# Kernel optimization log

Measured on AMD Instinct MI355X. Metric: run time of the kernel, lower is better.

The kernel has to match this reference:

```python
import jax, jax.numpy as jnp
import numpy as np

NODE_ATOM = 64   # nodes per graph (fixed by layer3 Linear(1*node_atom, n_h1))
N_H1 = 1024
DIM_OUT = 128
N_NODES = 524288          # 8192 graphs * 64 nodes
N_EDGES = 16777216        # avg degree 32
BN_EPS = 1e-5


def setup_inputs() -> dict:
    key = jax.random.key(0)
    ks = jax.random.split(key, 16)
    x = jax.random.normal(ks[0], (N_NODES, 1), dtype=jnp.float32)
    edge_attr = jax.random.uniform(ks[1], (N_EDGES, 1), dtype=jnp.float32)
    edge_index = jax.random.randint(ks[2], (2, N_EDGES), 0, N_NODES, dtype=jnp.int64)
    # CGConv gated MLP params: lin_f, lin_s : Linear(2*1+1=3 -> 1)
    cg_wf = jax.random.normal(ks[3], (1, 3), dtype=jnp.float32) * 0.5
    cg_bf = jax.random.normal(ks[4], (1,), dtype=jnp.float32) * 0.1
    cg_ws = jax.random.normal(ks[5], (1, 3), dtype=jnp.float32) * 0.5
    cg_bs = jax.random.normal(ks[6], (1,), dtype=jnp.float32) * 0.1
    # GCNConv(1,1)
    gcn_w = jax.random.normal(ks[7], (1, 1), dtype=jnp.float32)
    gcn_b = jax.random.normal(ks[8], (1,), dtype=jnp.float32) * 0.1
    # MLP head
    l3_w = jax.random.normal(ks[9], (N_H1, NODE_ATOM), dtype=jnp.float32) / np.sqrt(NODE_ATOM)
    l3_b = jax.random.normal(ks[10], (N_H1,), dtype=jnp.float32) * 0.1
    bn_gamma = jnp.ones((N_H1,), dtype=jnp.float32)
    bn_beta = jnp.zeros((N_H1,), dtype=jnp.float32)
    l4_w = jax.random.normal(ks[11], (DIM_OUT, N_H1), dtype=jnp.float32) / np.sqrt(N_H1)
    l4_b = jax.random.normal(ks[12], (DIM_OUT,), dtype=jnp.float32) * 0.1
    return {"x": x, "edge_attr": edge_attr, "cg_wf": cg_wf, "cg_bf": cg_bf,
            "cg_ws": cg_ws, "cg_bs": cg_bs, "gcn_w": gcn_w, "gcn_b": gcn_b,
            "l3_w": l3_w, "l3_b": l3_b, "bn_gamma": bn_gamma, "bn_beta": bn_beta,
            "l4_w": l4_w, "l4_b": l4_b, "edge_index": edge_index}


def reference(x, edge_attr, cg_wf, cg_bf, cg_ws, cg_bs, gcn_w, gcn_b,
              l3_w, l3_b, bn_gamma, bn_beta, l4_w, l4_b, edge_index):
    n = x.shape[0]
    src = edge_index[0]  # x_j (message source)
    dst = edge_index[1]  # x_i (aggregation target)

    # ---- CGConv: z = [x_i, x_j, e]; msg = sigmoid(Wf z) * softplus(Ws z); out = x + sum_j msg
    z = jnp.concatenate([x[dst], x[src], edge_attr], axis=-1)      # [E,3]
    msg = jax.nn.sigmoid(z @ cg_wf.T + cg_bf) * jax.nn.softplus(z @ cg_ws.T + cg_bs)
    h = x + jax.ops.segment_sum(msg, dst, num_segments=n)
    h = jax.nn.relu(h)  # dropout in eval mode = identity

    # ---- GCNConv(1,1, add_self_loops=False), edge_attr used as edge_weight
    w = edge_attr[:, 0]
    deg = jax.ops.segment_sum(w, dst, num_segments=n)
    dinv = jnp.where(deg > 0, 1.0 / jnp.sqrt(jnp.maximum(deg, 1e-12)), 0.0)
    norm = dinv[src] * w * dinv[dst]                               # [E]
    hw = h @ gcn_w.T                                               # [N,1]
    h = jax.ops.segment_sum(norm[:, None] * hw[src], dst, num_segments=n) + gcn_b
    h = jax.nn.relu(h)

    # ---- to_dense_batch (uniform sorted batch) + transpose + flatten == reshape [B, node_atom]
    b = n // NODE_ATOM
    h = h.reshape(b, NODE_ATOM)

    # ---- MLP head: Linear -> BatchNorm1d (eval: running mean 0, var 1) -> relu -> Linear -> relu
    h = h @ l3_w.T + l3_b
    h = bn_gamma * h / jnp.sqrt(1.0 + BN_EPS) + bn_beta
    h = jax.nn.relu(h)
    h = jax.nn.relu(h @ l4_w.T + l4_b)
    return h
```

## Files before the change

kernel.cpp:

```cpp
#include <hip/hip_runtime.h>
#include <math.h>

#define N_NODES 524288
#define N_EDGES 16777216
#define H1      1024
#define DOUT    128

#define NB        128
#define BSH       12
#define NODES_PB  4096
#define EPB       8192
#define NBLK      (N_EDGES / EPB)
#define CAP       139264
#define PWG       8

__device__ __forceinline__ float sigmoid_f(float v) {
    return 1.0f / (1.0f + __expf(-v));
}
__device__ __forceinline__ float softplus_f(float v) {
    return fmaxf(v, 0.0f) + log1pf(__expf(-fabsf(v)));
}


__global__ __launch_bounds__(1024) void a1_bin4(
    const int* __restrict__ ei, const float* __restrict__ ea,
    int* __restrict__ gcur,
    uint2* __restrict__ pkw_g)
{
    __shared__ int cnt[NB];
    __shared__ int gpos[NB];
    const int c = blockIdx.x, t = threadIdx.x;

    const int vi0 = c * 2048 + t;
    const int vi1 = vi0 + 1024;
    const int4 s4a = ((const int4*)ei)[vi0];
    const int4 s4b = ((const int4*)ei)[vi1];
    const int4 d4a = ((const int4*)(ei + N_EDGES))[vi0];
    const int4 d4b = ((const int4*)(ei + N_EDGES))[vi1];
    const float4 w4a = ((const float4*)ea)[vi0];
    const float4 w4b = ((const float4*)ea)[vi1];
    int srcs[8], dsts[8];
    float ws[8];
    srcs[0]=s4a.x; srcs[1]=s4a.y; srcs[2]=s4a.z; srcs[3]=s4a.w;
    srcs[4]=s4b.x; srcs[5]=s4b.y; srcs[6]=s4b.z; srcs[7]=s4b.w;
    dsts[0]=d4a.x; dsts[1]=d4a.y; dsts[2]=d4a.z; dsts[3]=d4a.w;
    dsts[4]=d4b.x; dsts[5]=d4b.y; dsts[6]=d4b.z; dsts[7]=d4b.w;
    ws[0]=w4a.x; ws[1]=w4a.y; ws[2]=w4a.z; ws[3]=w4a.w;
    ws[4]=w4b.x; ws[5]=w4b.y; ws[6]=w4b.z; ws[7]=w4b.w;

    if (t < NB) cnt[t] = 0;
    __syncthreads();

    int rank[8];
#pragma unroll
    for (int q = 0; q < 8; ++q)
        rank[q] = atomicAdd(&cnt[dsts[q] >> BSH], 1);
    __syncthreads();

    if (t < NB) gpos[t] = atomicAdd(&gcur[t * 16], cnt[t]);
    __syncthreads();

#pragma unroll
    for (int q = 0; q < 8; ++q) {
        const int dst = dsts[q];
        const int b = dst >> BSH;
        const size_t slot = (size_t)b * CAP + gpos[b] + rank[q];
        const unsigned int pk = ((unsigned int)srcs[q] << 12) |
                                (unsigned int)(dst & (NODES_PB - 1));
        pkw_g[slot] = make_uint2(pk, __float_as_uint(ws[q]));
    }
}

__global__ __launch_bounds__(512) void b1_accum(
    const uint2* __restrict__ pkw_g, const int* __restrict__ gcur,
    const float* __restrict__ x,
    const float* __restrict__ cg_wf, const float* __restrict__ cg_bf,
    const float* __restrict__ cg_ws, const float* __restrict__ cg_bs,
    float* __restrict__ part1)
{
    __shared__ float lm[NODES_PB];
    __shared__ float ld[NODES_PB];
    const int b = blockIdx.x / PWG, p = blockIdx.x % PWG;
    for (int i = threadIdx.x; i < NODES_PB; i += 512) { lm[i] = 0.0f; ld[i] = 0.0f; }
    __syncthreads();
    const float wf0 = cg_wf[0], wf1 = cg_wf[1], wf2 = cg_wf[2], bf = cg_bf[0];
    const float s0c = cg_ws[0], s1c = cg_ws[1], s2c = cg_ws[2], bsc = cg_bs[0];
    const float* xb = x + (size_t)b * NODES_PB;
    const int tot = gcur[b * 16];
    const int per = (((tot + PWG - 1) / PWG) + 1) & ~1;
    const int s0 = p * per;
    const int s1 = min(tot, s0 + per);
    const uint2* base = pkw_g + (size_t)b * CAP;
    if (s1 > s0) {
        const int npair = (s1 - s0) >> 1;
        const uint4* v4 = (const uint4*)(base + s0);
#pragma unroll 2
        for (int k = threadIdx.x; k < npair; k += 512) {
            const uint4 r = v4[k];
            const int dl0 = r.x & (NODES_PB - 1), src0 = r.x >> BSH;
            const int dl1 = r.z & (NODES_PB - 1), src1 = r.z >> BSH;
            const float w0 = __uint_as_float(r.y), w1 = __uint_as_float(r.w);
            const float xs0 = x[src0], xs1 = x[src1];
            const float xd0 = xb[dl0], xd1 = xb[dl1];
            const float f0 = fmaf(wf0, xd0, fmaf(wf1, xs0, fmaf(wf2, w0, bf)));
            const float g0 = fmaf(s0c, xd0, fmaf(s1c, xs0, fmaf(s2c, w0, bsc)));
            const float f1 = fmaf(wf0, xd1, fmaf(wf1, xs1, fmaf(wf2, w1, bf)));
            const float g1 = fmaf(s0c, xd1, fmaf(s1c, xs1, fmaf(s2c, w1, bsc)));
            const float m0 = sigmoid_f(f0) * softplus_f(g0);
            const float m1 = sigmoid_f(f1) * softplus_f(g1);
            atomicAdd(&lm[dl0], m0);
            atomicAdd(&ld[dl0], w0);
            atomicAdd(&lm[dl1], m1);
            atomicAdd(&ld[dl1], w1);
        }
        for (int k = s0 + (npair << 1) + (int)threadIdx.x; k < s1; k += 512) {
            const uint2 v = base[k];
            const int dl = v.x & (NODES_PB - 1);
            const int src = v.x >> BSH;
            const float w = __uint_as_float(v.y);
            const float xs = x[src], xd = xb[dl];
            const float f = fmaf(wf0, xd, fmaf(wf1, xs, fmaf(wf2, w, bf)));
            const float g = fmaf(s0c, xd, fmaf(s1c, xs, fmaf(s2c, w, bsc)));
            atomicAdd(&lm[dl], sigmoid_f(f) * softplus_f(g));
            atomicAdd(&ld[dl], w);
        }
    }
    __syncthreads();
    float* pm = part1 + (size_t)(b * PWG + p) * NODES_PB;
    float* pd = part1 + (size_t)NB * PWG * NODES_PB + (size_t)(b * PWG + p) * NODES_PB;
    for (int k = threadIdx.x; k < NODES_PB; k += 512) { pm[k] = lm[k]; pd[k] = ld[k]; }
}

__global__ __launch_bounds__(256) void c1_nodemid(
    const float* __restrict__ part1, const float* __restrict__ x,
    const float* __restrict__ gcn_w,
    float* __restrict__ dinv, float* __restrict__ a)
{
    const int n = blockIdx.x * 256 + threadIdx.x;
    const int b = n >> BSH, dl = n & (NODES_PB - 1);
    const float* pm = part1 + (size_t)b * PWG * NODES_PB + dl;
    const float* pd = part1 + (size_t)NB * PWG * NODES_PB + (size_t)b * PWG * NODES_PB + dl;
    float m = 0.0f, d = 0.0f;
#pragma unroll
    for (int p = 0; p < PWG; ++p) {
        m += pm[(size_t)p * NODES_PB];
        d += pd[(size_t)p * NODES_PB];
    }
    const float h = fmaxf(x[n] + m, 0.0f);
    const float di = (d > 0.0f) ? (1.0f / sqrtf(fmaxf(d, 1e-12f))) : 0.0f;
    dinv[n] = di;
    a[n] = di * h * gcn_w[0];
}

__global__ __launch_bounds__(512) void b2_accum(
    const uint2* __restrict__ pkw_g, const int* __restrict__ gcur,
    const float* __restrict__ a, float* __restrict__ part2)
{
    __shared__ float ls[NODES_PB];
    const int b = blockIdx.x / PWG, p = blockIdx.x % PWG;
    for (int i = threadIdx.x; i < NODES_PB; i += 512) ls[i] = 0.0f;
    __syncthreads();
    const int tot = gcur[b * 16];
    const int per = (((tot + PWG - 1) / PWG) + 1) & ~1;
    const int s0 = p * per;
    const int s1 = min(tot, s0 + per);
    const uint2* base = pkw_g + (size_t)b * CAP;
    if (s1 > s0) {
        const int npair = (s1 - s0) >> 1;
        const uint4* v4 = (const uint4*)(base + s0);
#pragma unroll 2
        for (int k = threadIdx.x; k < npair; k += 512) {
            const uint4 r = v4[k];
            const float a0 = a[r.x >> BSH];
            const float a1 = a[r.z >> BSH];
            atomicAdd(&ls[r.x & (NODES_PB - 1)], a0 * __uint_as_float(r.y));
            atomicAdd(&ls[r.z & (NODES_PB - 1)], a1 * __uint_as_float(r.w));
        }
        for (int k = s0 + (npair << 1) + (int)threadIdx.x; k < s1; k += 512) {
            const uint2 v = base[k];
            atomicAdd(&ls[v.x & (NODES_PB - 1)], a[v.x >> BSH] * __uint_as_float(v.y));
        }
    }
    __syncthreads();
    float* ps = part2 + (size_t)(b * PWG + p) * NODES_PB;
    for (int k = threadIdx.x; k < NODES_PB; k += 512) ps[k] = ls[k];
}

__global__ __launch_bounds__(256) void c2_nodefin(
    const float* __restrict__ part2, const float* __restrict__ dinv,
    const float* __restrict__ gcn_b, float* __restrict__ hfin)
{
    const int n = blockIdx.x * 256 + threadIdx.x;
    const int b = n >> BSH, dl = n & (NODES_PB - 1);
    const float* ps = part2 + (size_t)b * PWG * NODES_PB + dl;
    float s = 0.0f;
#pragma unroll
    for (int p = 0; p < PWG; ++p) s += ps[(size_t)p * NODES_PB];
    hfin[n] = fmaxf(fmaf(dinv[n], s, gcn_b[0]), 0.0f);
}


__global__ __launch_bounds__(256) void edge_pass1(
    const int* __restrict__ ei, const float* __restrict__ ea,
    const float* __restrict__ x,
    const float* __restrict__ cg_wf, const float* __restrict__ cg_bf,
    const float* __restrict__ cg_ws, const float* __restrict__ cg_bs,
    float* __restrict__ msg_sum, float* __restrict__ deg)
{
    const float wf0 = cg_wf[0], wf1 = cg_wf[1], wf2 = cg_wf[2], bf = cg_bf[0];
    const float s0 = cg_ws[0], s1 = cg_ws[1], s2 = cg_ws[2], bs = cg_bs[0];
    const int t = blockIdx.x * 256 + threadIdx.x;
    const int4 src4 = ((const int4*)ei)[t];
    const int4 dst4 = ((const int4*)(ei + N_EDGES))[t];
    const float4 w4 = ((const float4*)ea)[t];
    const int* sp = (const int*)&src4;
    const int* dp = (const int*)&dst4;
    const float* wp = (const float*)&w4;
#pragma unroll
    for (int q = 0; q < 4; ++q) {
        const int src = sp[q], dst = dp[q];
        const float w = wp[q];
        const float xs = x[src], xd = x[dst];
        const float f = fmaf(wf0, xd, fmaf(wf1, xs, fmaf(wf2, w, bf)));
        const float s = fmaf(s0, xd, fmaf(s1, xs, fmaf(s2, w, bs)));
        const float msg = sigmoid_f(f) * softplus_f(s);
        unsafeAtomicAdd(&msg_sum[dst], msg);
        unsafeAtomicAdd(&deg[dst], w);
    }
}

__global__ __launch_bounds__(256) void node_mid(
    const float* __restrict__ x, const float* __restrict__ msg_sum,
    float* __restrict__ deg_dinv, float* __restrict__ a,
    const float* __restrict__ gcn_w)
{
    const int i = blockIdx.x * 256 + threadIdx.x;
    const float gw = gcn_w[0];
    const float h = fmaxf(x[i] + msg_sum[i], 0.0f);
    const float d = deg_dinv[i];
    const float dinv = (d > 0.0f) ? (1.0f / sqrtf(fmaxf(d, 1e-12f))) : 0.0f;
    deg_dinv[i] = dinv;
    a[i] = dinv * h * gw;
}

__global__ __launch_bounds__(256) void edge_pass2(
    const int* __restrict__ ei, const float* __restrict__ ea,
    const float* __restrict__ a, float* __restrict__ s)
{
    const int t = blockIdx.x * 256 + threadIdx.x;
    const int4 src4 = ((const int4*)ei)[t];
    const int4 dst4 = ((const int4*)(ei + N_EDGES))[t];
    const float4 w4 = ((const float4*)ea)[t];
    const int* sp = (const int*)&src4;
    const int* dp = (const int*)&dst4;
    const float* wp = (const float*)&w4;
#pragma unroll
    for (int q = 0; q < 4; ++q)
        unsafeAtomicAdd(&s[dp[q]], a[sp[q]] * wp[q]);
}

__global__ __launch_bounds__(256) void node_fin(
    const float* __restrict__ dinv, const float* __restrict__ s,
    const float* __restrict__ gcn_b, float* __restrict__ hfin)
{
    const int i = blockIdx.x * 256 + threadIdx.x;
    hfin[i] = fmaxf(fmaf(dinv[i], s[i], gcn_b[0]), 0.0f);
}


__global__ __launch_bounds__(256) void fold_bn(
    const float* __restrict__ l3_w, const float* __restrict__ l3_b,
    const float* __restrict__ g, const float* __restrict__ be,
    float* __restrict__ w3f, float* __restrict__ b3f)
{
    const int idx = blockIdx.x * 256 + threadIdx.x;
    const int j = idx >> 6, k = idx & 63;
    const float invs = 1.0f / sqrtf(1.0f + 1e-5f);
    const float sc = g[j] * invs;
    w3f[idx] = l3_w[idx] * sc;
    if (k == 0) b3f[j] = fmaf(l3_b[j], sc, be[j]);
}

__global__ __launch_bounds__(256) void gemm1(
    const float* __restrict__ A, const float* __restrict__ W,
    const float* __restrict__ bias, float* __restrict__ C)
{
    __shared__ float As[64][68];
    __shared__ float Ws[64][68];
    const int bj = blockIdx.x, bi = blockIdx.y;
    const int t = threadIdx.x;
#pragma unroll
    for (int q2 = 0; q2 < 4; ++q2) {
        const int idx = t + 256 * q2;
        const int r = idx >> 4, c = idx & 15;
        const float4 va = *(const float4*)(A + (size_t)(bi * 64 + r) * 64 + c * 4);
        const float4 vw = *(const float4*)(W + (size_t)(bj * 64 + r) * 64 + c * 4);
        As[c*4+0][r] = va.x; As[c*4+1][r] = va.y; As[c*4+2][r] = va.z; As[c*4+3][r] = va.w;
        Ws[c*4+0][r] = vw.x; Ws[c*4+1][r] = vw.y; Ws[c*4+2][r] = vw.z; Ws[c*4+3][r] = vw.w;
    }
    __syncthreads();
    const int tx = t & 15, ty = t >> 4;
    const int i0 = ty * 4, j0 = tx * 4;
    float acc[4][4] = {};
#pragma unroll 16
    for (int k = 0; k < 64; ++k) {
        const float4 av = *(const float4*)&As[k][i0];
        const float4 wv = *(const float4*)&Ws[k][j0];
        const float* ap = (const float*)&av;
        const float* wp = (const float*)&wv;
#pragma unroll
        for (int ii = 0; ii < 4; ++ii)
#pragma unroll
            for (int jj = 0; jj < 4; ++jj)
                acc[ii][jj] = fmaf(ap[ii], wp[jj], acc[ii][jj]);
    }
    const int gj = bj * 64 + j0;
    const float4 bv = *(const float4*)(bias + gj);
#pragma unroll
    for (int ii = 0; ii < 4; ++ii) {
        const int gi = bi * 64 + i0 + ii;
        float4 o;
        o.x = fmaxf(acc[ii][0] + bv.x, 0.0f);
        o.y = fmaxf(acc[ii][1] + bv.y, 0.0f);
        o.z = fmaxf(acc[ii][2] + bv.z, 0.0f);
        o.w = fmaxf(acc[ii][3] + bv.w, 0.0f);
        *(float4*)(C + (size_t)gi * H1 + gj) = o;
    }
}

__global__ __launch_bounds__(256) void gemm2(
    const float* __restrict__ H, const float* __restrict__ W,
    const float* __restrict__ bias, float* __restrict__ O)
{
    __shared__ float Hs[64][36];
    __shared__ float Ws[64][132];
    const int bi = blockIdx.x;
    const int t = threadIdx.x;
    const int tx = t & 31, ty = t >> 5;
    const int i0 = ty * 4, j0 = tx * 4;
    float acc[4][4] = {};
    for (int kc = 0; kc < H1; kc += 64) {
#pragma unroll
        for (int q2 = 0; q2 < 2; ++q2) {
            const int idx = t + 256 * q2;
            const int r = idx >> 4, c = idx & 15;
            const float4 v = *(const float4*)(H + (size_t)(bi * 32 + r) * H1 + kc + c * 4);
            Hs[c*4+0][r] = v.x; Hs[c*4+1][r] = v.y; Hs[c*4+2][r] = v.z; Hs[c*4+3][r] = v.w;
        }
#pragma unroll
        for (int q2 = 0; q2 < 8; ++q2) {
            const int idx = t + 256 * q2;
            const int r = idx >> 4, c = idx & 15;
            const float4 v = *(const float4*)(W + (size_t)r * H1 + kc + c * 4);
            Ws[c*4+0][r] = v.x; Ws[c*4+1][r] = v.y; Ws[c*4+2][r] = v.z; Ws[c*4+3][r] = v.w;
        }
        __syncthreads();
#pragma unroll 16
        for (int k = 0; k < 64; ++k) {
            const float4 hv = *(const float4*)&Hs[k][i0];
            const float4 wv = *(const float4*)&Ws[k][j0];
            const float* hp = (const float*)&hv;
            const float* wp = (const float*)&wv;
#pragma unroll
            for (int ii = 0; ii < 4; ++ii)
#pragma unroll
                for (int jj = 0; jj < 4; ++jj)
                    acc[ii][jj] = fmaf(hp[ii], wp[jj], acc[ii][jj]);
        }
        __syncthreads();
    }
    const float4 bv = *(const float4*)(bias + j0);
#pragma unroll
    for (int ii = 0; ii < 4; ++ii) {
        const int gi = bi * 32 + i0 + ii;
        float4 o;
        o.x = fmaxf(acc[ii][0] + bv.x, 0.0f);
        o.y = fmaxf(acc[ii][1] + bv.y, 0.0f);
        o.z = fmaxf(acc[ii][2] + bv.z, 0.0f);
        o.w = fmaxf(acc[ii][3] + bv.w, 0.0f);
        *(float4*)(O + (size_t)gi * DOUT + j0) = o;
    }
}


extern "C" void kernel_launch(void* const* d_in, const int* in_sizes, int n_in,
                              void* d_out, int out_size, void* d_ws, size_t ws_size,
                              hipStream_t stream) {
    const float* x     = (const float*)d_in[0];
    const float* ea    = (const float*)d_in[1];
    const float* cg_wf = (const float*)d_in[2];
    const float* cg_bf = (const float*)d_in[3];
    const float* cg_ws = (const float*)d_in[4];
    const float* cg_bs = (const float*)d_in[5];
    const float* gcn_w = (const float*)d_in[6];
    const float* gcn_b = (const float*)d_in[7];
    const float* l3_w  = (const float*)d_in[8];
    const float* l3_b  = (const float*)d_in[9];
    const float* bn_g  = (const float*)d_in[10];
    const float* bn_b  = (const float*)d_in[11];
    const float* l4_w  = (const float*)d_in[12];
    const float* l4_b  = (const float*)d_in[13];
    const int*   ei    = (const int*)d_in[14];
    float* out = (float*)d_out;
    char* ws = (char*)d_ws;

    const size_t off_pkw   = 0;
    const size_t off_gcur  = off_pkw + (size_t)NB * CAP * 8;
    const size_t off_p1    = off_gcur + 8192;
    const size_t off_p2    = off_p1 + (size_t)NB * PWG * NODES_PB * 2 * 4;
    const size_t off_dinv  = off_p2 + (size_t)NB * PWG * NODES_PB * 4;
    const size_t off_a     = off_dinv + (size_t)N_NODES * 4;
    const size_t off_hfin  = off_a + (size_t)N_NODES * 4;
    const size_t off_h3    = off_hfin + (size_t)N_NODES * 4;
    const size_t off_w3    = off_h3 + (size_t)8192 * H1 * 4;
    const size_t off_b3    = off_w3 + (size_t)H1 * 64 * 4;
    const size_t required  = off_b3 + (size_t)H1 * 4;

    if (ws_size >= required) {
        uint2* pkw   = (uint2*)(ws + off_pkw);
        int*   gcur  = (int*)(ws + off_gcur);
        float* p1    = (float*)(ws + off_p1);
        float* p2    = (float*)(ws + off_p2);
        float* dinv  = (float*)(ws + off_dinv);
        float* a     = (float*)(ws + off_a);
        float* hfin  = (float*)(ws + off_hfin);
        float* h3    = (float*)(ws + off_h3);
        float* w3    = (float*)(ws + off_w3);
        float* b3    = (float*)(ws + off_b3);

        hipMemsetAsync(gcur, 0, 8192, stream);
        fold_bn<<<256, 256, 0, stream>>>(l3_w, l3_b, bn_g, bn_b, w3, b3);
        a1_bin4<<<NBLK, 1024, 0, stream>>>(ei, ea, gcur, pkw);
        b1_accum<<<NB * PWG, 512, 0, stream>>>(pkw, gcur, x,
                                               cg_wf, cg_bf, cg_ws, cg_bs, p1);
        c1_nodemid<<<N_NODES / 256, 256, 0, stream>>>(p1, x, gcn_w, dinv, a);
        b2_accum<<<NB * PWG, 512, 0, stream>>>(pkw, gcur, a, p2);
        c2_nodefin<<<N_NODES / 256, 256, 0, stream>>>(p2, dinv, gcn_b, hfin);
        gemm1<<<dim3(16, 128), 256, 0, stream>>>(hfin, w3, b3, h3);
        gemm2<<<256, 256, 0, stream>>>(h3, l4_w, l4_b, out);
    } else {
        float* buf_msg  = (float*)(ws + 0);
        float* buf_deg  = (float*)(ws + (size_t)2097152);
        float* buf_a    = (float*)(ws + (size_t)4194304);
        float* buf_hfin = (float*)(ws + (size_t)6291456);
        float* buf_h3   = (float*)(ws + (size_t)8388608);
        float* buf_w3   = (float*)(ws + (size_t)41943040);
        float* buf_b3   = (float*)(ws + (size_t)42205184);

        hipMemsetAsync(buf_msg, 0, (size_t)N_NODES * 4, stream);
        hipMemsetAsync(buf_deg, 0, (size_t)N_NODES * 4, stream);
        fold_bn<<<256, 256, 0, stream>>>(l3_w, l3_b, bn_g, bn_b, buf_w3, buf_b3);
        edge_pass1<<<N_EDGES / 4 / 256, 256, 0, stream>>>(
            ei, ea, x, cg_wf, cg_bf, cg_ws, cg_bs, buf_msg, buf_deg);
        node_mid<<<N_NODES / 256, 256, 0, stream>>>(x, buf_msg, buf_deg, buf_a, gcn_w);
        hipMemsetAsync(buf_msg, 0, (size_t)N_NODES * 4, stream);
        edge_pass2<<<N_EDGES / 4 / 256, 256, 0, stream>>>(ei, ea, buf_a, buf_msg);
        node_fin<<<N_NODES / 256, 256, 0, stream>>>(buf_deg, buf_msg, gcn_b, buf_hfin);
        gemm1<<<dim3(16, 128), 256, 0, stream>>>(buf_hfin, buf_w3, buf_b3, buf_h3);
        gemm2<<<256, 256, 0, stream>>>(buf_h3, l4_w, l4_b, out);
    }
}
```

Baseline: 683.9 us.

## Compute CGConv messages during edge binning and unroll accumulate loads

Moves the CGConv gated-message computation into the binning kernel, which already reads src/dst/weight. It gathers x[src] and x[dst] there and writes a per-slot message array next to the packed edge records. The first accumulate kernel then only does shared-memory atomics on precomputed messages, with no random x gathers or transcendental math. Both accumulate kernels now batch four vector loads per thread before their atomics to raise memory-level parallelism. The cost is an extra 4-byte-per-edge message array written and read back, and more workspace (msg overlaps the later buffers, with a fallback to the old path when workspace is too small).

```diff
diff --git a/kernel.cpp b/kernel.cpp
--- a/kernel.cpp
+++ b/kernel.cpp
@@ -21,6 +21,129 @@
     return fmaxf(v, 0.0f) + log1pf(__expf(-fabsf(v)));
 }
 
+
+__global__ __launch_bounds__(1024) void a1_bin4m(
+    const int* __restrict__ ei, const float* __restrict__ ea,
+    const float* __restrict__ x,
+    const float* __restrict__ cg_wf, const float* __restrict__ cg_bf,
+    const float* __restrict__ cg_ws, const float* __restrict__ cg_bs,
+    int* __restrict__ gcur,
+    uint2* __restrict__ pkw_g,
+    float* __restrict__ msg_g)
+{
+    __shared__ int cnt[NB];
+    __shared__ int gpos[NB];
+    const int c = blockIdx.x, t = threadIdx.x;
+
+    const float wf0 = cg_wf[0], wf1 = cg_wf[1], wf2 = cg_wf[2], bf = cg_bf[0];
+    const float s0c = cg_ws[0], s1c = cg_ws[1], s2c = cg_ws[2], bsc = cg_bs[0];
+
+    const int vi0 = c * 2048 + t;
+    const int vi1 = vi0 + 1024;
+    const int4 s4a = ((const int4*)ei)[vi0];
+    const int4 s4b = ((const int4*)ei)[vi1];
+    const int4 d4a = ((const int4*)(ei + N_EDGES))[vi0];
+    const int4 d4b = ((const int4*)(ei + N_EDGES))[vi1];
+    const float4 w4a = ((const float4*)ea)[vi0];
+    const float4 w4b = ((const float4*)ea)[vi1];
+    int srcs[8], dsts[8];
+    float ws[8];
+    srcs[0]=s4a.x; srcs[1]=s4a.y; srcs[2]=s4a.z; srcs[3]=s4a.w;
+    srcs[4]=s4b.x; srcs[5]=s4b.y; srcs[6]=s4b.z; srcs[7]=s4b.w;
+    dsts[0]=d4a.x; dsts[1]=d4a.y; dsts[2]=d4a.z; dsts[3]=d4a.w;
+    dsts[4]=d4b.x; dsts[5]=d4b.y; dsts[6]=d4b.z; dsts[7]=d4b.w;
+    ws[0]=w4a.x; ws[1]=w4a.y; ws[2]=w4a.z; ws[3]=w4a.w;
+    ws[4]=w4b.x; ws[5]=w4b.y; ws[6]=w4b.z; ws[7]=w4b.w;
+
+    float xs[8], xd[8];
+#pragma unroll
+    for (int q = 0; q < 8; ++q) xs[q] = x[srcs[q]];
+#pragma unroll
+    for (int q = 0; q < 8; ++q) xd[q] = x[dsts[q]];
+
+    if (t < NB) cnt[t] = 0;
+    __syncthreads();
+
+    int rank[8];
+#pragma unroll
+    for (int q = 0; q < 8; ++q)
+        rank[q] = atomicAdd(&cnt[dsts[q] >> BSH], 1);
+    __syncthreads();
+
+    if (t < NB) gpos[t] = atomicAdd(&gcur[t * 16], cnt[t]);
+    __syncthreads();
+
+    float msg[8];
+#pragma unroll
+    for (int q = 0; q < 8; ++q) {
+        const float f = fmaf(wf0, xd[q], fmaf(wf1, xs[q], fmaf(wf2, ws[q], bf)));
+        const float g = fmaf(s0c, xd[q], fmaf(s1c, xs[q], fmaf(s2c, ws[q], bsc)));
+        msg[q] = sigmoid_f(f) * softplus_f(g);
+    }
+
+#pragma unroll
+    for (int q = 0; q < 8; ++q) {
+        const int dst = dsts[q];
+        const int b = dst >> BSH;
+        const size_t slot = (size_t)b * CAP + gpos[b] + rank[q];
+        const unsigned int pk = ((unsigned int)srcs[q] << 12) |
+                                (unsigned int)(dst & (NODES_PB - 1));
+        pkw_g[slot] = make_uint2(pk, __float_as_uint(ws[q]));
+        msg_g[slot] = msg[q];
+    }
+}
+
+__global__ __launch_bounds__(512) void b1_accum_m(
+    const uint2* __restrict__ pkw_g, const float* __restrict__ msg_g,
+    const int* __restrict__ gcur,
+    float* __restrict__ part1)
+{
+    __shared__ float lm[NODES_PB];
+    __shared__ float ld[NODES_PB];
+    const int b = blockIdx.x / PWG, p = blockIdx.x % PWG;
+    for (int i = threadIdx.x; i < NODES_PB; i += 512) { lm[i] = 0.0f; ld[i] = 0.0f; }
+    __syncthreads();
+    const int tot = gcur[b * 16];
+    const int per = (((tot + PWG - 1) / PWG) + 1) & ~1;
+    const int s0 = p * per;
+    const int s1 = min(tot, s0 + per);
+    const uint2* base = pkw_g + (size_t)b * CAP;
+    const float* msgb = msg_g + (size_t)b * CAP;
+    if (s1 > s0) {
+        const int npair = (s1 - s0) >> 1;
+        const uint4*  v4 = (const uint4*)(base + s0);
+        const float2* m2 = (const float2*)(msgb + s0);
+        for (int k = (int)threadIdx.x; k < npair; k += 2048) {
+            uint4 r[4]; float2 mm[4];
+#pragma unroll
+            for (int u = 0; u < 4; ++u) {
+                const int kk = k + u * 512;
+                const int ks = (kk < npair) ? kk : k;
+                r[u]  = v4[ks];
+                mm[u] = m2[ks];
+            }
+#pragma unroll
+            for (int u = 0; u < 4; ++u) {
+                if (k + u * 512 < npair) {
+                    atomicAdd(&lm[r[u].x & (NODES_PB - 1)], mm[u].x);
+                    atomicAdd(&ld[r[u].x & (NODES_PB - 1)], __uint_as_float(r[u].y));
+                    atomicAdd(&lm[r[u].z & (NODES_PB - 1)], mm[u].y);
+                    atomicAdd(&ld[r[u].z & (NODES_PB - 1)], __uint_as_float(r[u].w));
+                }
+            }
+        }
+        for (int k = s0 + (((s1 - s0) >> 1) << 1) + (int)threadIdx.x; k < s1; k += 512) {
+            const uint2 v = base[k];
+            const int dl = v.x & (NODES_PB - 1);
+            atomicAdd(&lm[dl], msgb[k]);
+            atomicAdd(&ld[dl], __uint_as_float(v.y));
+        }
+    }
+    __syncthreads();
+    float* pm = part1 + (size_t)(b * PWG + p) * NODES_PB;
+    float* pd = part1 + (size_t)NB * PWG * NODES_PB + (size_t)(b * PWG + p) * NODES_PB;
+    for (int k = threadIdx.x; k < NODES_PB; k += 512) { pm[k] = lm[k]; pd[k] = ld[k]; }
+}
 
 __global__ __launch_bounds__(1024) void a1_bin4(
     const int* __restrict__ ei, const float* __restrict__ ea,
@@ -168,15 +291,28 @@
     if (s1 > s0) {
         const int npair = (s1 - s0) >> 1;
         const uint4* v4 = (const uint4*)(base + s0);
-#pragma unroll 2
-        for (int k = threadIdx.x; k < npair; k += 512) {
-            const uint4 r = v4[k];
-            const float a0 = a[r.x >> BSH];
-            const float a1 = a[r.z >> BSH];
-            atomicAdd(&ls[r.x & (NODES_PB - 1)], a0 * __uint_as_float(r.y));
-            atomicAdd(&ls[r.z & (NODES_PB - 1)], a1 * __uint_as_float(r.w));
-        }
-        for (int k = s0 + (npair << 1) + (int)threadIdx.x; k < s1; k += 512) {
+        for (int k = (int)threadIdx.x; k < npair; k += 2048) {
+            uint4 r[4];
+#pragma unroll
+            for (int u = 0; u < 4; ++u) {
+                const int kk = k + u * 512;
+                r[u] = v4[(kk < npair) ? kk : k];
+            }
+            float av[8];
+#pragma unroll
+            for (int u = 0; u < 4; ++u) {
+                av[2*u]   = a[r[u].x >> BSH];
+                av[2*u+1] = a[r[u].z >> BSH];
+            }
+#pragma unroll
+            for (int u = 0; u < 4; ++u) {
+                if (k + u * 512 < npair) {
+                    atomicAdd(&ls[r[u].x & (NODES_PB - 1)], av[2*u]   * __uint_as_float(r[u].y));
+                    atomicAdd(&ls[r[u].z & (NODES_PB - 1)], av[2*u+1] * __uint_as_float(r[u].w));
+                }
+            }
+        }
+        for (int k = s0 + (((s1 - s0) >> 1) << 1) + (int)threadIdx.x; k < s1; k += 512) {
             const uint2 v = base[k];
             atomicAdd(&ls[v.x & (NODES_PB - 1)], a[v.x >> BSH] * __uint_as_float(v.y));
         }
@@ -407,6 +543,20 @@
     const size_t off_pkw   = 0;
     const size_t off_gcur  = off_pkw + (size_t)NB * CAP * 8;
     const size_t off_p1    = off_gcur + 8192;
+
+    const size_t off_msg   = off_p1 + (size_t)NB * PWG * NODES_PB * 2 * 4;
+    const size_t msg_bytes = (size_t)NB * CAP * 4;
+    const size_t off_p2n   = off_msg;
+    const size_t off_dinvn = off_p2n + (size_t)NB * PWG * NODES_PB * 4;
+    const size_t off_an    = off_dinvn + (size_t)N_NODES * 4;
+    const size_t off_hfinn = off_an + (size_t)N_NODES * 4;
+    const size_t off_h3n   = off_hfinn + (size_t)N_NODES * 4;
+    const size_t off_w3n   = off_h3n + (size_t)8192 * H1 * 4;
+    const size_t off_b3n   = off_w3n + (size_t)H1 * 64 * 4;
+    const size_t end_tail  = off_b3n + (size_t)H1 * 4;
+    const size_t required_new = (off_msg + msg_bytes > end_tail) ? (off_msg + msg_bytes)
+                                                                 : end_tail;
+
     const size_t off_p2    = off_p1 + (size_t)NB * PWG * NODES_PB * 2 * 4;
     const size_t off_dinv  = off_p2 + (size_t)NB * PWG * NODES_PB * 4;
     const size_t off_a     = off_dinv + (size_t)N_NODES * 4;
@@ -416,7 +566,30 @@
     const size_t off_b3    = off_w3 + (size_t)H1 * 64 * 4;
     const size_t required  = off_b3 + (size_t)H1 * 4;
 
-    if (ws_size >= required) {
+    if (ws_size >= required_new) {
+        uint2* pkw   = (uint2*)(ws + off_pkw);
+        int*   gcur  = (int*)(ws + off_gcur);
+        float* p1    = (float*)(ws + off_p1);
+        float* msg   = (float*)(ws + off_msg);
+        float* p2    = (float*)(ws + off_p2n);
+        float* dinv  = (float*)(ws + off_dinvn);
+        float* a     = (float*)(ws + off_an);
+        float* hfin  = (float*)(ws + off_hfinn);
+        float* h3    = (float*)(ws + off_h3n);
+        float* w3    = (float*)(ws + off_w3n);
+        float* b3    = (float*)(ws + off_b3n);
+
+        hipMemsetAsync(gcur, 0, 8192, stream);
+        a1_bin4m<<<NBLK, 1024, 0, stream>>>(ei, ea, x, cg_wf, cg_bf, cg_ws, cg_bs,
+                                            gcur, pkw, msg);
+        b1_accum_m<<<NB * PWG, 512, 0, stream>>>(pkw, msg, gcur, p1);
+        fold_bn<<<256, 256, 0, stream>>>(l3_w, l3_b, bn_g, bn_b, w3, b3);
+        c1_nodemid<<<N_NODES / 256, 256, 0, stream>>>(p1, x, gcn_w, dinv, a);
+        b2_accum<<<NB * PWG, 512, 0, stream>>>(pkw, gcur, a, p2);
+        c2_nodefin<<<N_NODES / 256, 256, 0, stream>>>(p2, dinv, gcn_b, hfin);
+        gemm1<<<dim3(16, 128), 256, 0, stream>>>(hfin, w3, b3, h3);
+        gemm2<<<256, 256, 0, stream>>>(h3, l4_w, l4_b, out);
+    } else if (ws_size >= required) {
         uint2* pkw   = (uint2*)(ws + off_pkw);
         int*   gcur  = (int*)(ws + off_gcur);
         float* p1    = (float*)(ws + off_p1);
```

Result: slower. 878.5 us (+28.4%).

## Compute CGConv messages during binning and stage SoA edge buckets through LDS

Applied to the files above, without the earlier changes.

The binning kernel now gathers x for source and destination and computes the gated CGConv message per edge. It locally sorts edges by bucket in shared memory with a prefix scan, then writes packed index, weight and message as three coalesced structure-of-arrays streams. The first accumulation pass becomes a pure LDS scatter of precomputed messages and weights. The second pass reads the SoA streams with 4-wide vector loads and more gathers in flight per thread. This removes random x gathers and transcendental work from the accumulation pass and replaces scattered 8-byte global writes with coalesced ones, at the cost of writing and reading an extra 4 bytes of message per edge. Workspace buffers are aliased over the message region once it is no longer needed.

```diff
diff --git a/kernel.cpp b/kernel.cpp
--- a/kernel.cpp
+++ b/kernel.cpp
@@ -9,7 +9,7 @@
 #define NB        128
 #define BSH       12
 #define NODES_PB  4096
-#define EPB       8192
+#define EPB       4096
 #define NBLK      (N_EDGES / EPB)
 #define CAP       139264
 #define PWG       8
@@ -22,17 +22,31 @@
 }
 
 
-__global__ __launch_bounds__(1024) void a1_bin4(
+__global__ __launch_bounds__(512) void a1_stage(
     const int* __restrict__ ei, const float* __restrict__ ea,
+    const float* __restrict__ x,
+    const float* __restrict__ cg_wf, const float* __restrict__ cg_bf,
+    const float* __restrict__ cg_ws, const float* __restrict__ cg_bs,
     int* __restrict__ gcur,
-    uint2* __restrict__ pkw_g)
-{
+    unsigned int* __restrict__ upk_g,
+    float* __restrict__ uw_g,
+    float* __restrict__ umsg_g)
+{
+    __shared__ unsigned int lpk[EPB];
+    __shared__ float        lw[EPB];
+    __shared__ float        lmsg[EPB];
     __shared__ int cnt[NB];
+    __shared__ int scan[NB];
+    __shared__ int boff[NB];
     __shared__ int gpos[NB];
+
     const int c = blockIdx.x, t = threadIdx.x;
 
-    const int vi0 = c * 2048 + t;
-    const int vi1 = vi0 + 1024;
+    const float wf0 = cg_wf[0], wf1 = cg_wf[1], wf2 = cg_wf[2], bf = cg_bf[0];
+    const float s0c = cg_ws[0], s1c = cg_ws[1], s2c = cg_ws[2], bsc = cg_bs[0];
+
+    const int vi0 = c * 1024 + t;
+    const int vi1 = vi0 + 512;
     const int4 s4a = ((const int4*)ei)[vi0];
     const int4 s4b = ((const int4*)ei)[vi1];
     const int4 d4a = ((const int4*)(ei + N_EDGES))[vi0];
@@ -48,6 +62,12 @@
     ws[0]=w4a.x; ws[1]=w4a.y; ws[2]=w4a.z; ws[3]=w4a.w;
     ws[4]=w4b.x; ws[5]=w4b.y; ws[6]=w4b.z; ws[7]=w4b.w;
 
+    float xs[8], xd[8];
+#pragma unroll
+    for (int q = 0; q < 8; ++q) xs[q] = x[srcs[q]];
+#pragma unroll
+    for (int q = 0; q < 8; ++q) xd[q] = x[dsts[q]];
+
     if (t < NB) cnt[t] = 0;
     __syncthreads();
 
@@ -57,25 +77,57 @@
         rank[q] = atomicAdd(&cnt[dsts[q] >> BSH], 1);
     __syncthreads();
 
-    if (t < NB) gpos[t] = atomicAdd(&gcur[t * 16], cnt[t]);
+    if (t < NB) scan[t] = cnt[t];
+    __syncthreads();
+    for (int o = 1; o < NB; o <<= 1) {
+        int v = 0;
+        if (t < NB && t >= o) v = scan[t - o];
+        __syncthreads();
+        if (t < NB) scan[t] += v;
+        __syncthreads();
+    }
+    if (t < NB) {
+        boff[t] = scan[t] - cnt[t];
+        gpos[t] = atomicAdd(&gcur[t * 16], cnt[t]);
+    }
+
+    float msg[8];
+#pragma unroll
+    for (int q = 0; q < 8; ++q) {
+        const float f = fmaf(wf0, xd[q], fmaf(wf1, xs[q], fmaf(wf2, ws[q], bf)));
+        const float g = fmaf(s0c, xd[q], fmaf(s1c, xs[q], fmaf(s2c, ws[q], bsc)));
+        msg[q] = sigmoid_f(f) * softplus_f(g);
+    }
     __syncthreads();
 
 #pragma unroll
     for (int q = 0; q < 8; ++q) {
         const int dst = dsts[q];
         const int b = dst >> BSH;
-        const size_t slot = (size_t)b * CAP + gpos[b] + rank[q];
-        const unsigned int pk = ((unsigned int)srcs[q] << 12) |
-                                (unsigned int)(dst & (NODES_PB - 1));
-        pkw_g[slot] = make_uint2(pk, __float_as_uint(ws[q]));
-    }
-}
-
-__global__ __launch_bounds__(512) void b1_accum(
-    const uint2* __restrict__ pkw_g, const int* __restrict__ gcur,
-    const float* __restrict__ x,
-    const float* __restrict__ cg_wf, const float* __restrict__ cg_bf,
-    const float* __restrict__ cg_ws, const float* __restrict__ cg_bs,
+        const int pos = boff[b] + rank[q];
+        lpk[pos]  = ((unsigned int)srcs[q] << 12) |
+                    (unsigned int)(dst & (NODES_PB - 1));
+        lw[pos]   = ws[q];
+        lmsg[pos] = msg[q];
+    }
+    __syncthreads();
+
+    const int wv = t >> 6, lane = t & 63;
+    for (int b = wv; b < NB; b += 8) {
+        const int n   = cnt[b];
+        const int off = boff[b];
+        const size_t gbase = (size_t)b * CAP + gpos[b];
+        for (int i = lane; i < n; i += 64) {
+            upk_g[gbase + i]  = lpk[off + i];
+            uw_g[gbase + i]   = lw[off + i];
+            umsg_g[gbase + i] = lmsg[off + i];
+        }
+    }
+}
+
+__global__ __launch_bounds__(512) void b1_accum_m(
+    const unsigned int* __restrict__ upk, const float* __restrict__ uw,
+    const float* __restrict__ umsg, const int* __restrict__ gcur,
     float* __restrict__ part1)
 {
     __shared__ float lm[NODES_PB];
@@ -83,46 +135,35 @@
     const int b = blockIdx.x / PWG, p = blockIdx.x % PWG;
     for (int i = threadIdx.x; i < NODES_PB; i += 512) { lm[i] = 0.0f; ld[i] = 0.0f; }
     __syncthreads();
-    const float wf0 = cg_wf[0], wf1 = cg_wf[1], wf2 = cg_wf[2], bf = cg_bf[0];
-    const float s0c = cg_ws[0], s1c = cg_ws[1], s2c = cg_ws[2], bsc = cg_bs[0];
-    const float* xb = x + (size_t)b * NODES_PB;
     const int tot = gcur[b * 16];
-    const int per = (((tot + PWG - 1) / PWG) + 1) & ~1;
+    const int per = (((tot + PWG - 1) / PWG) + 3) & ~3;
     const int s0 = p * per;
     const int s1 = min(tot, s0 + per);
-    const uint2* base = pkw_g + (size_t)b * CAP;
     if (s1 > s0) {
-        const int npair = (s1 - s0) >> 1;
-        const uint4* v4 = (const uint4*)(base + s0);
-#pragma unroll 2
-        for (int k = threadIdx.x; k < npair; k += 512) {
-            const uint4 r = v4[k];
-            const int dl0 = r.x & (NODES_PB - 1), src0 = r.x >> BSH;
-            const int dl1 = r.z & (NODES_PB - 1), src1 = r.z >> BSH;
-            const float w0 = __uint_as_float(r.y), w1 = __uint_as_float(r.w);
-            const float xs0 = x[src0], xs1 = x[src1];
-            const float xd0 = xb[dl0], xd1 = xb[dl1];
-            const float f0 = fmaf(wf0, xd0, fmaf(wf1, xs0, fmaf(wf2, w0, bf)));
-            const float g0 = fmaf(s0c, xd0, fmaf(s1c, xs0, fmaf(s2c, w0, bsc)));
-            const float f1 = fmaf(wf0, xd1, fmaf(wf1, xs1, fmaf(wf2, w1, bf)));
-            const float g1 = fmaf(s0c, xd1, fmaf(s1c, xs1, fmaf(s2c, w1, bsc)));
-            const float m0 = sigmoid_f(f0) * softplus_f(g0);
-            const float m1 = sigmoid_f(f1) * softplus_f(g1);
-            atomicAdd(&lm[dl0], m0);
-            atomicAdd(&ld[dl0], w0);
-            atomicAdd(&lm[dl1], m1);
-            atomicAdd(&ld[dl1], w1);
-        }
-        for (int k = s0 + (npair << 1) + (int)threadIdx.x; k < s1; k += 512) {
-            const uint2 v = base[k];
-            const int dl = v.x & (NODES_PB - 1);
-            const int src = v.x >> BSH;
-            const float w = __uint_as_float(v.y);
-            const float xs = x[src], xd = xb[dl];
-            const float f = fmaf(wf0, xd, fmaf(wf1, xs, fmaf(wf2, w, bf)));
-            const float g = fmaf(s0c, xd, fmaf(s1c, xs, fmaf(s2c, w, bsc)));
-            atomicAdd(&lm[dl], sigmoid_f(f) * softplus_f(g));
-            atomicAdd(&ld[dl], w);
+        const unsigned int* pk = upk + (size_t)b * CAP + s0;
+        const float* wv = uw   + (size_t)b * CAP + s0;
+        const float* mv = umsg + (size_t)b * CAP + s0;
+        const int n  = s1 - s0;
+        const int nq = n >> 2;
+        const uint4*  pk4 = (const uint4*)pk;
+        const float4* w4  = (const float4*)wv;
+        const float4* m4  = (const float4*)mv;
+        for (int k = (int)threadIdx.x; k < nq; k += 512) {
+            const uint4  a4 = pk4[k];
+            const float4 ww = w4[k];
+            const float4 mm = m4[k];
+            atomicAdd(&lm[a4.x & (NODES_PB - 1)], mm.x);
+            atomicAdd(&ld[a4.x & (NODES_PB - 1)], ww.x);
+            atomicAdd(&lm[a4.y & (NODES_PB - 1)], mm.y);
+            atomicAdd(&ld[a4.y & (NODES_PB - 1)], ww.y);
+            atomicAdd(&lm[a4.z & (NODES_PB - 1)], mm.z);
+            atomicAdd(&ld[a4.z & (NODES_PB - 1)], ww.z);
+            atomicAdd(&lm[a4.w & (NODES_PB - 1)], mm.w);
+            atomicAdd(&ld[a4.w & (NODES_PB - 1)], ww.w);
+        }
+        for (int k = (nq << 2) + (int)threadIdx.x; k < n; k += 512) {
+            atomicAdd(&lm[pk[k] & (NODES_PB - 1)], mv[k]);
+            atomicAdd(&ld[pk[k] & (NODES_PB - 1)], wv[k]);
         }
     }
     __syncthreads();
@@ -152,33 +193,51 @@
     a[n] = di * h * gcn_w[0];
 }
 
-__global__ __launch_bounds__(512) void b2_accum(
-    const uint2* __restrict__ pkw_g, const int* __restrict__ gcur,
-    const float* __restrict__ a, float* __restrict__ part2)
+__global__ __launch_bounds__(512) void b2_accum_soa(
+    const unsigned int* __restrict__ upk, const float* __restrict__ uw,
+    const int* __restrict__ gcur, const float* __restrict__ a,
+    float* __restrict__ part2)
 {
     __shared__ float ls[NODES_PB];
     const int b = blockIdx.x / PWG, p = blockIdx.x % PWG;
     for (int i = threadIdx.x; i < NODES_PB; i += 512) ls[i] = 0.0f;
     __syncthreads();
     const int tot = gcur[b * 16];
-    const int per = (((tot + PWG - 1) / PWG) + 1) & ~1;
+    const int per = (((tot + PWG - 1) / PWG) + 3) & ~3;
     const int s0 = p * per;
     const int s1 = min(tot, s0 + per);
-    const uint2* base = pkw_g + (size_t)b * CAP;
     if (s1 > s0) {
-        const int npair = (s1 - s0) >> 1;
-        const uint4* v4 = (const uint4*)(base + s0);
-#pragma unroll 2
-        for (int k = threadIdx.x; k < npair; k += 512) {
-            const uint4 r = v4[k];
-            const float a0 = a[r.x >> BSH];
-            const float a1 = a[r.z >> BSH];
-            atomicAdd(&ls[r.x & (NODES_PB - 1)], a0 * __uint_as_float(r.y));
-            atomicAdd(&ls[r.z & (NODES_PB - 1)], a1 * __uint_as_float(r.w));
-        }
-        for (int k = s0 + (npair << 1) + (int)threadIdx.x; k < s1; k += 512) {
-            const uint2 v = base[k];
-            atomicAdd(&ls[v.x & (NODES_PB - 1)], a[v.x >> BSH] * __uint_as_float(v.y));
+        const unsigned int* pk = upk + (size_t)b * CAP + s0;
+        const float* wv = uw + (size_t)b * CAP + s0;
+        const int n  = s1 - s0;
+        const int nq = n >> 2;
+        const uint4*  pk4 = (const uint4*)pk;
+        const float4* w4  = (const float4*)wv;
+        for (int k = (int)threadIdx.x; k < nq; k += 1024) {
+            const int k2 = k + 512;
+            const bool h2 = (k2 < nq);
+            const uint4  pa = pk4[k];
+            const float4 wa = w4[k];
+            const uint4  pb = pk4[h2 ? k2 : k];
+            const float4 wb = w4[h2 ? k2 : k];
+            const float g0 = a[pa.x >> 12], g1 = a[pa.y >> 12];
+            const float g2 = a[pa.z >> 12], g3 = a[pa.w >> 12];
+            const float g4 = a[pb.x >> 12], g5 = a[pb.y >> 12];
+            const float g6 = a[pb.z >> 12], g7 = a[pb.w >> 12];
+            atomicAdd(&ls[pa.x & (NODES_PB - 1)], g0 * wa.x);
+            atomicAdd(&ls[pa.y & (NODES_PB - 1)], g1 * wa.y);
+            atomicAdd(&ls[pa.z & (NODES_PB - 1)], g2 * wa.z);
+            atomicAdd(&ls[pa.w & (NODES_PB - 1)], g3 * wa.w);
+            if (h2) {
+                atomicAdd(&ls[pb.x & (NODES_PB - 1)], g4 * wb.x);
+                atomicAdd(&ls[pb.y & (NODES_PB - 1)], g5 * wb.y);
+                atomicAdd(&ls[pb.z & (NODES_PB - 1)], g6 * wb.z);
+                atomicAdd(&ls[pb.w & (NODES_PB - 1)], g7 * wb.w);
+            }
+        }
+        for (int k = (nq << 2) + (int)threadIdx.x; k < n; k += 512) {
+            const unsigned int v = pk[k];
+            atomicAdd(&ls[v & (NODES_PB - 1)], a[v >> 12] * wv[k]);
         }
     }
     __syncthreads();
@@ -404,20 +463,26 @@
     float* out = (float*)d_out;
     char* ws = (char*)d_ws;
 
-    const size_t off_pkw   = 0;
-    const size_t off_gcur  = off_pkw + (size_t)NB * CAP * 8;
-    const size_t off_p1    = off_gcur + 8192;
-    const size_t off_p2    = off_p1 + (size_t)NB * PWG * NODES_PB * 2 * 4;
-    const size_t off_dinv  = off_p2 + (size_t)NB * PWG * NODES_PB * 4;
-    const size_t off_a     = off_dinv + (size_t)N_NODES * 4;
-    const size_t off_hfin  = off_a + (size_t)N_NODES * 4;
-    const size_t off_h3    = off_hfin + (size_t)N_NODES * 4;
-    const size_t off_w3    = off_h3 + (size_t)8192 * H1 * 4;
-    const size_t off_b3    = off_w3 + (size_t)H1 * 64 * 4;
-    const size_t required  = off_b3 + (size_t)H1 * 4;
+    const size_t off_upk  = 0;
+    const size_t off_uw   = off_upk + (size_t)NB * CAP * 4;
+    const size_t off_umsg = off_uw  + (size_t)NB * CAP * 4;
+    const size_t off_gcur = off_umsg + (size_t)NB * CAP * 4;
+    const size_t off_p1   = off_gcur + 8192;
+    const size_t end_p1   = off_p1 + (size_t)NB * PWG * NODES_PB * 2 * 4;
+
+    const size_t off_p2   = off_umsg;
+    const size_t off_dinv = off_p2   + (size_t)NB * PWG * NODES_PB * 4;
+    const size_t off_a    = off_dinv + (size_t)N_NODES * 4;
+    const size_t off_hfin = off_a    + (size_t)N_NODES * 4;
+    const size_t off_h3   = off_hfin + (size_t)N_NODES * 4;
+    const size_t off_w3   = off_h3   + (size_t)8192 * H1 * 4;
+    const size_t off_b3   = off_w3   + (size_t)H1 * 64 * 4;
+    const size_t required = end_p1;
 
     if (ws_size >= required) {
-        uint2* pkw   = (uint2*)(ws + off_pkw);
+        unsigned int* upk = (unsigned int*)(ws + off_upk);
+        float* uw    = (float*)(ws + off_uw);
+        float* umsg  = (float*)(ws + off_umsg);
         int*   gcur  = (int*)(ws + off_gcur);
         float* p1    = (float*)(ws + off_p1);
         float* p2    = (float*)(ws + off_p2);
@@ -429,12 +494,12 @@
         float* b3    = (float*)(ws + off_b3);
 
         hipMemsetAsync(gcur, 0, 8192, stream);
+        a1_stage<<<NBLK, 512, 0, stream>>>(ei, ea, x, cg_wf, cg_bf, cg_ws, cg_bs,
+                                           gcur, upk, uw, umsg);
+        b1_accum_m<<<NB * PWG, 512, 0, stream>>>(upk, uw, umsg, gcur, p1);
         fold_bn<<<256, 256, 0, stream>>>(l3_w, l3_b, bn_g, bn_b, w3, b3);
-        a1_bin4<<<NBLK, 1024, 0, stream>>>(ei, ea, gcur, pkw);
-        b1_accum<<<NB * PWG, 512, 0, stream>>>(pkw, gcur, x,
-                                               cg_wf, cg_bf, cg_ws, cg_bs, p1);
         c1_nodemid<<<N_NODES / 256, 256, 0, stream>>>(p1, x, gcn_w, dinv, a);
-        b2_accum<<<NB * PWG, 512, 0, stream>>>(pkw, gcur, a, p2);
+        b2_accum_soa<<<NB * PWG, 512, 0, stream>>>(upk, uw, gcur, a, p2);
         c2_nodefin<<<N_NODES / 256, 256, 0, stream>>>(p2, dinv, gcn_b, hfin);
         gemm1<<<dim3(16, 128), 256, 0, stream>>>(hfin, w3, b3, h3);
         gemm2<<<256, 256, 0, stream>>>(h3, l4_w, l4_b, out);
```

Result: slower. 802.4 us (+17.3%).

## Stage binned edge records in LDS for coalesced global writes; widen accum loads

Applied to the files above, without the earlier changes.

The binning kernel now sorts each block's 8192 edge records by destination bucket in shared memory, using a prefix scan over bucket counts. It then copies each bucket's run to global memory contiguously, one wavefront per bucket, instead of scattering 8-byte records directly. This is meant to turn scattered stores into mostly coalesced stores. The two accumulation kernels also process four records per thread per iteration with two 16-byte loads, which raises memory-level parallelism. The cost is 64KB of LDS per block plus extra barriers for the scan, which may reduce occupancy of the binning kernel.

```diff
diff --git a/kernel.cpp b/kernel.cpp
--- a/kernel.cpp
+++ b/kernel.cpp
@@ -22,13 +22,17 @@
 }
 
 
-__global__ __launch_bounds__(1024) void a1_bin4(
+__global__ __launch_bounds__(1024) void a1_stage2(
     const int* __restrict__ ei, const float* __restrict__ ea,
     int* __restrict__ gcur,
-    uint2* __restrict__ pkw_g)
-{
+    uint2* __restrict__ urec)
+{
+    __shared__ uint2 lrec[EPB];
     __shared__ int cnt[NB];
+    __shared__ int scan[NB];
+    __shared__ int boff[NB];
     __shared__ int gpos[NB];
+
     const int c = blockIdx.x, t = threadIdx.x;
 
     const int vi0 = c * 2048 + t;
@@ -57,22 +61,46 @@
         rank[q] = atomicAdd(&cnt[dsts[q] >> BSH], 1);
     __syncthreads();
 
-    if (t < NB) gpos[t] = atomicAdd(&gcur[t * 16], cnt[t]);
+    if (t < NB) scan[t] = cnt[t];
+    __syncthreads();
+    for (int o = 1; o < NB; o <<= 1) {
+        int v = 0;
+        if (t < NB && t >= o) v = scan[t - o];
+        __syncthreads();
+        if (t < NB) scan[t] += v;
+        __syncthreads();
+    }
+    if (t < NB) {
+        boff[t] = scan[t] - cnt[t];
+        gpos[t] = atomicAdd(&gcur[t * 16], cnt[t]);
+    }
     __syncthreads();
 
 #pragma unroll
     for (int q = 0; q < 8; ++q) {
         const int dst = dsts[q];
         const int b = dst >> BSH;
-        const size_t slot = (size_t)b * CAP + gpos[b] + rank[q];
-        const unsigned int pk = ((unsigned int)srcs[q] << 12) |
-                                (unsigned int)(dst & (NODES_PB - 1));
-        pkw_g[slot] = make_uint2(pk, __float_as_uint(ws[q]));
+        lrec[boff[b] + rank[q]] =
+            make_uint2(((unsigned int)srcs[q] << 12) |
+                       (unsigned int)(dst & (NODES_PB - 1)),
+                       __float_as_uint(ws[q]));
+    }
+    __syncthreads();
+
+    const int wv = t >> 6, lane = t & 63;
+    const unsigned int* lw = (const unsigned int*)lrec;
+    unsigned int* gw = (unsigned int*)urec;
+    for (int b = wv; b < NB; b += 16) {
+        const int n2   = cnt[b] * 2;
+        const int loff = boff[b] * 2;
+        const size_t gbase = ((size_t)b * CAP + gpos[b]) * 2;
+        for (int i = lane; i < n2; i += 64)
+            gw[gbase + i] = lw[loff + i];
     }
 }
 
 __global__ __launch_bounds__(512) void b1_accum(
-    const uint2* __restrict__ pkw_g, const int* __restrict__ gcur,
+    const uint2* __restrict__ urec, const int* __restrict__ gcur,
     const float* __restrict__ x,
     const float* __restrict__ cg_wf, const float* __restrict__ cg_bf,
     const float* __restrict__ cg_ws, const float* __restrict__ cg_bs,
@@ -87,38 +115,52 @@
     const float s0c = cg_ws[0], s1c = cg_ws[1], s2c = cg_ws[2], bsc = cg_bs[0];
     const float* xb = x + (size_t)b * NODES_PB;
     const int tot = gcur[b * 16];
-    const int per = (((tot + PWG - 1) / PWG) + 1) & ~1;
+    const int per = (((tot + PWG - 1) / PWG) + 3) & ~3;
     const int s0 = p * per;
     const int s1 = min(tot, s0 + per);
-    const uint2* base = pkw_g + (size_t)b * CAP;
     if (s1 > s0) {
-        const int npair = (s1 - s0) >> 1;
-        const uint4* v4 = (const uint4*)(base + s0);
-#pragma unroll 2
-        for (int k = threadIdx.x; k < npair; k += 512) {
-            const uint4 r = v4[k];
-            const int dl0 = r.x & (NODES_PB - 1), src0 = r.x >> BSH;
-            const int dl1 = r.z & (NODES_PB - 1), src1 = r.z >> BSH;
-            const float w0 = __uint_as_float(r.y), w1 = __uint_as_float(r.w);
-            const float xs0 = x[src0], xs1 = x[src1];
-            const float xd0 = xb[dl0], xd1 = xb[dl1];
+        const uint2* base = urec + (size_t)b * CAP + s0;
+        const int n  = s1 - s0;
+        const int nq = n >> 2;
+        const uint4* v4 = (const uint4*)base;
+        for (int k = (int)threadIdx.x; k < nq; k += 512) {
+            const uint4 ra = v4[2 * k];
+            const uint4 rb = v4[2 * k + 1];
+            const int dl0 = ra.x & (NODES_PB - 1), sr0 = ra.x >> BSH;
+            const int dl1 = ra.z & (NODES_PB - 1), sr1 = ra.z >> BSH;
+            const int dl2 = rb.x & (NODES_PB - 1), sr2 = rb.x >> BSH;
+            const int dl3 = rb.z & (NODES_PB - 1), sr3 = rb.z >> BSH;
+            const float w0 = __uint_as_float(ra.y), w1 = __uint_as_float(ra.w);
+            const float w2 = __uint_as_float(rb.y), w3 = __uint_as_float(rb.w);
+            const float xs0 = x[sr0], xs1 = x[sr1], xs2 = x[sr2], xs3 = x[sr3];
+            const float xd0 = xb[dl0], xd1 = xb[dl1], xd2 = xb[dl2], xd3 = xb[dl3];
             const float f0 = fmaf(wf0, xd0, fmaf(wf1, xs0, fmaf(wf2, w0, bf)));
             const float g0 = fmaf(s0c, xd0, fmaf(s1c, xs0, fmaf(s2c, w0, bsc)));
             const float f1 = fmaf(wf0, xd1, fmaf(wf1, xs1, fmaf(wf2, w1, bf)));
             const float g1 = fmaf(s0c, xd1, fmaf(s1c, xs1, fmaf(s2c, w1, bsc)));
+            const float f2 = fmaf(wf0, xd2, fmaf(wf1, xs2, fmaf(wf2, w2, bf)));
+            const float g2 = fmaf(s0c, xd2, fmaf(s1c, xs2, fmaf(s2c, w2, bsc)));
+            const float f3 = fmaf(wf0, xd3, fmaf(wf1, xs3, fmaf(wf2, w3, bf)));
+            const float g3 = fmaf(s0c, xd3, fmaf(s1c, xs3, fmaf(s2c, w3, bsc)));
             const float m0 = sigmoid_f(f0) * softplus_f(g0);
             const float m1 = sigmoid_f(f1) * softplus_f(g1);
+            const float m2 = sigmoid_f(f2) * softplus_f(g2);
+            const float m3 = sigmoid_f(f3) * softplus_f(g3);
             atomicAdd(&lm[dl0], m0);
             atomicAdd(&ld[dl0], w0);
             atomicAdd(&lm[dl1], m1);
             atomicAdd(&ld[dl1], w1);
-        }
-        for (int k = s0 + (npair << 1) + (int)threadIdx.x; k < s1; k += 512) {
+            atomicAdd(&lm[dl2], m2);
+            atomicAdd(&ld[dl2], w2);
+            atomicAdd(&lm[dl3], m3);
+            atomicAdd(&ld[dl3], w3);
+        }
+        for (int k = (nq << 2) + (int)threadIdx.x; k < n; k += 512) {
             const uint2 v = base[k];
             const int dl = v.x & (NODES_PB - 1);
-            const int src = v.x >> BSH;
+            const int sr = v.x >> BSH;
             const float w = __uint_as_float(v.y);
-            const float xs = x[src], xd = xb[dl];
+            const float xs = x[sr], xd = xb[dl];
             const float f = fmaf(wf0, xd, fmaf(wf1, xs, fmaf(wf2, w, bf)));
             const float g = fmaf(s0c, xd, fmaf(s1c, xs, fmaf(s2c, w, bsc)));
             atomicAdd(&lm[dl], sigmoid_f(f) * softplus_f(g));
@@ -153,7 +195,7 @@
 }
 
 __global__ __launch_bounds__(512) void b2_accum(
-    const uint2* __restrict__ pkw_g, const int* __restrict__ gcur,
+    const uint2* __restrict__ urec, const int* __restrict__ gcur,
     const float* __restrict__ a, float* __restrict__ part2)
 {
     __shared__ float ls[NODES_PB];
@@ -161,22 +203,27 @@
     for (int i = threadIdx.x; i < NODES_PB; i += 512) ls[i] = 0.0f;
     __syncthreads();
     const int tot = gcur[b * 16];
-    const int per = (((tot + PWG - 1) / PWG) + 1) & ~1;
+    const int per = (((tot + PWG - 1) / PWG) + 3) & ~3;
     const int s0 = p * per;
     const int s1 = min(tot, s0 + per);
-    const uint2* base = pkw_g + (size_t)b * CAP;
     if (s1 > s0) {
-        const int npair = (s1 - s0) >> 1;
-        const uint4* v4 = (const uint4*)(base + s0);
-#pragma unroll 2
-        for (int k = threadIdx.x; k < npair; k += 512) {
-            const uint4 r = v4[k];
-            const float a0 = a[r.x >> BSH];
-            const float a1 = a[r.z >> BSH];
-            atomicAdd(&ls[r.x & (NODES_PB - 1)], a0 * __uint_as_float(r.y));
-            atomicAdd(&ls[r.z & (NODES_PB - 1)], a1 * __uint_as_float(r.w));
-        }
-        for (int k = s0 + (npair << 1) + (int)threadIdx.x; k < s1; k += 512) {
+        const uint2* base = urec + (size_t)b * CAP + s0;
+        const int n  = s1 - s0;
+        const int nq = n >> 2;
+        const uint4* v4 = (const uint4*)base;
+        for (int k = (int)threadIdx.x; k < nq; k += 512) {
+            const uint4 ra = v4[2 * k];
+            const uint4 rb = v4[2 * k + 1];
+            const float g0 = a[ra.x >> BSH];
+            const float g1 = a[ra.z >> BSH];
+            const float g2 = a[rb.x >> BSH];
+            const float g3 = a[rb.z >> BSH];
+            atomicAdd(&ls[ra.x & (NODES_PB - 1)], g0 * __uint_as_float(ra.y));
+            atomicAdd(&ls[ra.z & (NODES_PB - 1)], g1 * __uint_as_float(ra.w));
+            atomicAdd(&ls[rb.x & (NODES_PB - 1)], g2 * __uint_as_float(rb.y));
+            atomicAdd(&ls[rb.z & (NODES_PB - 1)], g3 * __uint_as_float(rb.w));
+        }
+        for (int k = (nq << 2) + (int)threadIdx.x; k < n; k += 512) {
             const uint2 v = base[k];
             atomicAdd(&ls[v.x & (NODES_PB - 1)], a[v.x >> BSH] * __uint_as_float(v.y));
         }
@@ -404,20 +451,20 @@
     float* out = (float*)d_out;
     char* ws = (char*)d_ws;
 
-    const size_t off_pkw   = 0;
-    const size_t off_gcur  = off_pkw + (size_t)NB * CAP * 8;
-    const size_t off_p1    = off_gcur + 8192;
-    const size_t off_p2    = off_p1 + (size_t)NB * PWG * NODES_PB * 2 * 4;
-    const size_t off_dinv  = off_p2 + (size_t)NB * PWG * NODES_PB * 4;
-    const size_t off_a     = off_dinv + (size_t)N_NODES * 4;
-    const size_t off_hfin  = off_a + (size_t)N_NODES * 4;
-    const size_t off_h3    = off_hfin + (size_t)N_NODES * 4;
-    const size_t off_w3    = off_h3 + (size_t)8192 * H1 * 4;
-    const size_t off_b3    = off_w3 + (size_t)H1 * 64 * 4;
-    const size_t required  = off_b3 + (size_t)H1 * 4;
+    const size_t off_rec  = 0;
+    const size_t off_gcur = off_rec + (size_t)NB * CAP * 8;
+    const size_t off_p1   = off_gcur + 8192;
+    const size_t off_p2   = off_p1 + (size_t)NB * PWG * NODES_PB * 2 * 4;
+    const size_t off_dinv = off_p2 + (size_t)NB * PWG * NODES_PB * 4;
+    const size_t off_a    = off_dinv + (size_t)N_NODES * 4;
+    const size_t off_hfin = off_a + (size_t)N_NODES * 4;
+    const size_t off_h3   = off_hfin + (size_t)N_NODES * 4;
+    const size_t off_w3   = off_h3 + (size_t)8192 * H1 * 4;
+    const size_t off_b3   = off_w3 + (size_t)H1 * 64 * 4;
+    const size_t required = off_b3 + (size_t)H1 * 4;
 
     if (ws_size >= required) {
-        uint2* pkw   = (uint2*)(ws + off_pkw);
+        uint2* urec  = (uint2*)(ws + off_rec);
         int*   gcur  = (int*)(ws + off_gcur);
         float* p1    = (float*)(ws + off_p1);
         float* p2    = (float*)(ws + off_p2);
@@ -430,11 +477,11 @@
 
         hipMemsetAsync(gcur, 0, 8192, stream);
         fold_bn<<<256, 256, 0, stream>>>(l3_w, l3_b, bn_g, bn_b, w3, b3);
-        a1_bin4<<<NBLK, 1024, 0, stream>>>(ei, ea, gcur, pkw);
-        b1_accum<<<NB * PWG, 512, 0, stream>>>(pkw, gcur, x,
+        a1_stage2<<<NBLK, 1024, 0, stream>>>(ei, ea, gcur, urec);
+        b1_accum<<<NB * PWG, 512, 0, stream>>>(urec, gcur, x,
                                                cg_wf, cg_bf, cg_ws, cg_bs, p1);
         c1_nodemid<<<N_NODES / 256, 256, 0, stream>>>(p1, x, gcn_w, dinv, a);
-        b2_accum<<<NB * PWG, 512, 0, stream>>>(pkw, gcur, a, p2);
+        b2_accum<<<NB * PWG, 512, 0, stream>>>(urec, gcur, a, p2);
         c2_nodefin<<<N_NODES / 256, 256, 0, stream>>>(p2, dinv, gcn_b, hfin);
         gemm1<<<dim3(16, 128), 256, 0, stream>>>(hfin, w3, b3, h3);
         gemm2<<<256, 256, 0, stream>>>(h3, l4_w, l4_b, out);
```

After: 668.9 us. 1.02x faster.
